# Performance work log

Measured on AMD Instinct MI355X. Metric: run time of the kernel, lower is better.

## Reference

```python
import jax, jax.numpy as jnp
import numpy as np

B, T, D, H = 2, 2048, 1024, 16
DH = D // H  # head dim = 64


def setup_inputs() -> dict:
    key = jax.random.key(0)
    ks = jax.random.split(key, 10)
    s = D ** -0.5
    inp = {
        "x": jax.random.normal(ks[0], (B, T, D), jnp.float32),
        "data_mask": jax.random.randint(ks[1], (B, T), 0, 2, jnp.int32),
        "Wq": jax.random.normal(ks[2], (D, D), jnp.float32) * s,
        "bq": jnp.zeros((D,), jnp.float32),
        "Wk": jax.random.normal(ks[3], (D, D), jnp.float32) * s,
        "bk": jnp.zeros((D,), jnp.float32),
        "Wv": jax.random.normal(ks[4], (D, D), jnp.float32) * s,
        "bv": jnp.zeros((D,), jnp.float32),
        "Wp": jax.random.normal(ks[5], (D, D), jnp.float32) * s,
        "bp": jnp.zeros((D,), jnp.float32),
    }
    return inp


def _split_heads(t):
    # [B, T, D] -> [B, H, T, DH]
    return jnp.swapaxes(t.reshape(B, T, H, DH), 1, 2)


def reference(x, data_mask, Wq, bq, Wk, bk, Wv, bv, Wp, bp):
    q = _split_heads(x @ Wq + bq)
    k = _split_heads(x @ Wk + bk)  # kv = x (self-attention)
    v = _split_heads(x @ Wv + bv)

    # combined mask: causal tri AND data_mask outer product -> [B, 1, T, T]
    dm = data_mask.astype(bool)
    causal = jnp.tril(jnp.ones((T, T), bool))
    mask = causal[None, None] & (dm[:, None, :, None] & dm[:, None, None, :])

    q = q * (DH ** -0.5)  # scale_logits
    scores = jnp.einsum('bhqd,bhkd->bhqk', q, k)  # [B, H, T, T]
    scores = jnp.where(mask, scores, -jnp.inf)
    weights = jax.nn.softmax(scores, axis=-1)
    weights = jnp.nan_to_num(weights)  # fully-masked rows -> 0
    o = jnp.einsum('bhqk,bhkd->bhqd', weights, v)

    # recover shape: [B, H, T, DH] -> [B, T, D]
    o = jnp.swapaxes(o, 1, 2).reshape(B, T, D)
    o = o @ Wp + bp

    # linear mask: multiply output by data_mask [B, T, 1]
    o = o * data_mask.astype(o.dtype)[..., None]
    return o
```

## Files before the change

kernel.cpp:

```cpp
#include <hip/hip_runtime.h>
#include <hip/hip_bf16.h>
#include <cstdint>
#include <cstddef>

#define Bb 2
#define Tt 2048
#define Dd 1024
#define Hh 16
#define DHh 64

using short8 = __attribute__((ext_vector_type(8))) short;
using f32x4  = __attribute__((ext_vector_type(4))) float;
typedef unsigned short u16;

__device__ __forceinline__ u16 f2bf(float f) {
    unsigned int u = __float_as_uint(f);
    u += 0x7fffu + ((u >> 16) & 1u);
    return (u16)(u >> 16);
}

__device__ __forceinline__ unsigned int pk2bf(float a, float b) {
    union { __hip_bfloat162 h; unsigned int u; } c;
    c.h = __float22bfloat162_rn(float2{a, b});
    return c.u;
}

__device__ __forceinline__ void gload16(const void* g, void* l) {
    __builtin_amdgcn_global_load_lds((const __attribute__((address_space(1))) void*)g,
                                     (__attribute__((address_space(3))) void*)l, 16, 0, 0);
}

__device__ __forceinline__ void gemm_bt_core(const u16* __restrict__ A, const u16* __restrict__ BT,
                                             int K, int m0, int n0,
                                             u16* As, u16* Bs, f32x4 acc[4][4]) {
    const int tid = threadIdx.x;
    const int w = tid >> 6, lane = tid & 63;
    const int lr = lane & 15, lg = lane >> 4;
    const int wr = w >> 1, wc = w & 1;
    const int arow = lane >> 2;
    const int acol = (lane & 3) * 8;
    for (int kk = 0; kk < K; kk += 32) {
        __syncthreads();
#pragma unroll
        for (int j = 0; j < 2; ++j) {
            int r0 = w * 32 + j * 16;
            gload16(A  + (size_t)(m0 + r0 + arow) * K + kk + acol, (char*)As + r0 * 64);
            gload16(BT + (size_t)(n0 + r0 + arow) * K + kk + acol, (char*)Bs + r0 * 64);
        }
        __syncthreads();
        short8 af[4], bfv[4];
#pragma unroll
        for (int m = 0; m < 4; ++m)
            af[m] = *(const short8*)((const char*)As + ((wr * 64 + m * 16 + lr) * 64 + lg * 16));
#pragma unroll
        for (int n = 0; n < 4; ++n)
            bfv[n] = *(const short8*)((const char*)Bs + ((wc * 64 + n * 16 + lr) * 64 + lg * 16));
#pragma unroll
        for (int m = 0; m < 4; ++m)
#pragma unroll
            for (int n = 0; n < 4; ++n)
                acc[m][n] = __builtin_amdgcn_mfma_f32_16x16x32_bf16(af[m], bfv[n], acc[m][n], 0, 0, 0);
    }
}

__global__ __launch_bounds__(256) void convert_x_k(const float4* __restrict__ x4,
                                                   ushort4* __restrict__ xb4, int n4,
                                                   const int* __restrict__ dmask,
                                                   float* __restrict__ dmb) {
    int i = blockIdx.x * 256 + threadIdx.x;
    if (i < n4) {
        float4 v = x4[i];
        ushort4 o;
        o.x = f2bf(v.x); o.y = f2bf(v.y); o.z = f2bf(v.z); o.w = f2bf(v.w);
        xb4[i] = o;
    }
    if (i < Bb * Tt) dmb[i] = dmask[i] ? 0.f : -15000.f;
}

__global__ void transpose_w_k(const float* __restrict__ Wq, const float* __restrict__ Wk,
                              const float* __restrict__ Wv, const float* __restrict__ Wp,
                              u16* __restrict__ wt) {
    __shared__ float tile[32][33];
    const int z = blockIdx.z;
    const float* W = (z == 0) ? Wq : (z == 1) ? Wk : (z == 2) ? Wv : Wp;
    const int n0 = blockIdx.x * 32, k0 = blockIdx.y * 32;
    const int tx = threadIdx.x, ty = threadIdx.y;
#pragma unroll
    for (int j = 0; j < 4; ++j)
        tile[ty + j * 8][tx] = W[(size_t)(k0 + ty + j * 8) * Dd + n0 + tx];
    __syncthreads();
    u16* outp = wt + (size_t)z * Dd * Dd;
#pragma unroll
    for (int j = 0; j < 4; ++j)
        outp[(size_t)(n0 + ty + j * 8) * Dd + k0 + tx] = f2bf(tile[tx][ty + j * 8]);
}

__global__ __launch_bounds__(256) void qkv_gemm_k(const u16* __restrict__ xb, const u16* __restrict__ wt,
        const float* __restrict__ bq, const float* __restrict__ bk, const float* __restrict__ bv,
        u16* __restrict__ Qg, u16* __restrict__ Kg, u16* __restrict__ VTg) {
    __shared__ alignas(16) u16 As[128 * 32];
    __shared__ alignas(16) u16 Bs[128 * 32];
    f32x4 acc[4][4];
    const f32x4 vzero = {0.f, 0.f, 0.f, 0.f};
#pragma unroll
    for (int m = 0; m < 4; ++m)
#pragma unroll
        for (int n = 0; n < 4; ++n) acc[m][n] = vzero;
    const int m0 = blockIdx.y * 128, n0 = blockIdx.x * 128;
    gemm_bt_core(xb, wt, 1024, m0, n0, As, Bs, acc);
    const int tid = threadIdx.x, w = tid >> 6, lane = tid & 63, lr = lane & 15, lg = lane >> 4;
    const int wr = w >> 1, wc = w & 1;
    const int sec = n0 >> 10;
    const float* bias = (sec == 0) ? bq : (sec == 1) ? bk : bv;
    u16* dst = (sec == 0) ? Qg : (sec == 1) ? Kg : VTg;
    const float qscale = (sec == 0) ? 0.125f * 1.4426950408889634f : 1.0f;
#pragma unroll
    for (int n = 0; n < 4; ++n) {
        int gn = n0 + wc * 64 + n * 16 + lr;
        int j = gn & 1023;
        float bj = bias[j];
        int h = j >> 6, dh = j & 63;
#pragma unroll
        for (int m = 0; m < 4; ++m) {
            int gmb = m0 + wr * 64 + m * 16 + 4 * lg;
#pragma unroll
            for (int i = 0; i < 4; ++i) {
                int gm = gmb + i;
                int b = gm >> 11, t = gm & 2047;
                float v = (acc[m][n][i] + bj) * qscale;
                size_t off;
                if (sec < 2) off = (((size_t)(b * Hh + h)) * Tt + t) * DHh + dh;
                else {
                    int kt2 = t >> 7, a = t & 127;
                    int ks2 = a >> 5, r = a & 31;
                    int pos = ks2 * 32 + ((r & 15) >> 2) * 8 + ((r >> 4) & 1) * 4 + (r & 3);
                    int chunkp = (pos >> 3) ^ (dh & 7);
                    off = (((size_t)(b * Hh + h) * 16 + kt2) * 64 + dh) * 128 + chunkp * 8 + (pos & 7);
                }
                dst[off] = f2bf(v);
            }
        }
    }
}

__global__ __launch_bounds__(256, 4) void attn_k(const u16* __restrict__ Qg, const u16* __restrict__ Kg,
        const u16* __restrict__ VTg, const float* __restrict__ dmb, u16* __restrict__ Og) {
    __shared__ alignas(16) u16 Ks[128 * 64];
    __shared__ alignas(16) u16 Vs[64 * 128];
    const int bh = blockIdx.x;
    const int qb = (int)gridDim.y - 1 - (int)blockIdx.y;
    const int b = bh >> 4, h = bh & 15;
    const int tid = threadIdx.x, w = tid >> 6, lane = tid & 63;
    const int lr = lane & 15, lg = lane >> 4;
    const int q0 = qb * 64 + w * 16;
    const int qrow = q0 + lr;
    const u16* Qbase = Qg + ((size_t)bh * Tt + q0) * DHh;
    short8 qf0 = *(const short8*)(Qbase + lr * DHh + lg * 8);
    short8 qf1 = *(const short8*)(Qbase + lr * DHh + 32 + lg * 8);
    const f32x4 vzero = {0.f, 0.f, 0.f, 0.f};
    const short8 ones8 = {(short)0x3F80, (short)0x3F80, (short)0x3F80, (short)0x3F80,
                          (short)0x3F80, (short)0x3F80, (short)0x3F80, (short)0x3F80};
    f32x4 o[4];
#pragma unroll
    for (int n = 0; n < 4; ++n) o[n] = vzero;
    f32x4 acc_l = vzero;
    const int ktiles = (qb * 64 + 63) / 128 + 1;
    char* KsB = (char*)Ks; char* VsB = (char*)Vs;

    for (int kt = 0; kt < ktiles; ++kt) {
        const int kbase = kt * 128;
        __syncthreads();
#pragma unroll
        for (int j = 0; j < 4; ++j) {
            int r0 = w * 32 + j * 8;
            int r = r0 + (lane >> 3);
            int cs = (lane & 7) ^ (r & 7);
            gload16(Kg + ((size_t)bh * Tt + kbase + r) * DHh + cs * 8, KsB + r0 * 128);
        }
        {
            const u16* vsrc = VTg + (((size_t)bh * 16 + kt) * 8192) + w * 2048 + lane * 8;
#pragma unroll
            for (int j = 0; j < 4; ++j)
                gload16(vsrc + j * 512, VsB + w * 4096 + j * 1024);
        }
        __syncthreads();
        f32x4 s[8];
        const float* bb = dmb + (size_t)b * Tt + kbase + 4 * lg;
#pragma unroll
        for (int nf = 0; nf < 8; ++nf) {
            int r = nf * 16 + lr;
            short8 k0v = *(const short8*)(KsB + r * 128 + (((0 + lg) ^ (r & 7)) << 4));
            short8 k1v = *(const short8*)(KsB + r * 128 + (((4 + lg) ^ (r & 7)) << 4));
            f32x4 cin = *(const f32x4*)(bb + nf * 16);
            f32x4 t0 = __builtin_amdgcn_mfma_f32_16x16x32_bf16(k0v, qf0, cin, 0, 0, 0);
            s[nf] = __builtin_amdgcn_mfma_f32_16x16x32_bf16(k1v, qf1, t0, 0, 0, 0);
        }
        if (kbase + 127 > q0) {
#pragma unroll
            for (int nf = 0; nf < 8; ++nf) {
                int tk = kbase + 16 * nf + 4 * lg;
#pragma unroll
                for (int i = 0; i < 4; ++i)
                    if (tk + i > qrow) s[nf][i] -= 15000.f;
            }
        }
#pragma unroll
        for (int ks = 0; ks < 4; ++ks) {
            union { uint4 u; short8 sv; } pf;
            pf.u.x = pk2bf(exp2f(s[2 * ks][0]), exp2f(s[2 * ks][1]));
            pf.u.y = pk2bf(exp2f(s[2 * ks][2]), exp2f(s[2 * ks][3]));
            pf.u.z = pk2bf(exp2f(s[2 * ks + 1][0]), exp2f(s[2 * ks + 1][1]));
            pf.u.w = pk2bf(exp2f(s[2 * ks + 1][2]), exp2f(s[2 * ks + 1][3]));
            acc_l = __builtin_amdgcn_mfma_f32_16x16x32_bf16(ones8, pf.sv, acc_l, 0, 0, 0);
#pragma unroll
            for (int n = 0; n < 4; ++n) {
                int rv = n * 16 + lr;
                short8 vf = *(const short8*)(VsB + rv * 256 + ((((ks * 4 + lg)) ^ (rv & 7)) << 4));
                o[n] = __builtin_amdgcn_mfma_f32_16x16x32_bf16(vf, pf.sv, o[n], 0, 0, 0);
            }
        }
    }
    float l = acc_l[0];
    float inv = l > 0.f ? 1.0f / l : 0.f;
#pragma unroll
    for (int n = 0; n < 4; ++n) {
        uint2 pw;
        pw.x = pk2bf(o[n][0] * inv, o[n][1] * inv);
        pw.y = pk2bf(o[n][2] * inv, o[n][3] * inv);
        *(uint2*)(Og + ((size_t)(b * Tt + qrow)) * Dd + h * DHh + n * 16 + 4 * lg) = pw;
    }
}

__global__ __launch_bounds__(256) void out_gemm_k(const u16* __restrict__ Og, const u16* __restrict__ wpt,
        const float* __restrict__ bp, const int* __restrict__ dmask, float* __restrict__ out) {
    __shared__ alignas(16) u16 As[128 * 32];
    __shared__ alignas(16) u16 Bs[128 * 32];
    f32x4 acc[4][4];
    const f32x4 vzero = {0.f, 0.f, 0.f, 0.f};
#pragma unroll
    for (int m = 0; m < 4; ++m)
#pragma unroll
        for (int n = 0; n < 4; ++n) acc[m][n] = vzero;
    const int m0 = blockIdx.y * 128, n0 = blockIdx.x * 128;
    gemm_bt_core(Og, wpt, 1024, m0, n0, As, Bs, acc);
    const int tid = threadIdx.x, w = tid >> 6, lane = tid & 63, lr = lane & 15, lg = lane >> 4;
    const int wr = w >> 1, wc = w & 1;
#pragma unroll
    for (int n = 0; n < 4; ++n) {
        int gn = n0 + wc * 64 + n * 16 + lr;
        float bj = bp[gn];
#pragma unroll
        for (int m = 0; m < 4; ++m) {
            int gmb = m0 + wr * 64 + m * 16 + 4 * lg;
#pragma unroll
            for (int i = 0; i < 4; ++i) {
                int gm = gmb + i;
                float dmv = (float)dmask[gm];
                out[(size_t)gm * Dd + gn] = (acc[m][n][i] + bj) * dmv;
            }
        }
    }
}

extern "C" void kernel_launch(void* const* d_in, const int* in_sizes, int n_in,
                              void* d_out, int out_size, void* d_ws, size_t ws_size,
                              hipStream_t stream) {
    const float* x   = (const float*)d_in[0];
    const int*  dmask = (const int*)d_in[1];
    const float* Wq = (const float*)d_in[2];
    const float* bq = (const float*)d_in[3];
    const float* Wk = (const float*)d_in[4];
    const float* bk = (const float*)d_in[5];
    const float* Wv = (const float*)d_in[6];
    const float* bv = (const float*)d_in[7];
    const float* Wp = (const float*)d_in[8];
    const float* bp = (const float*)d_in[9];
    float* out = (float*)d_out;
    char* ws = (char*)d_ws;
    u16* xb  = (u16*)(ws);
    u16* wt  = (u16*)(ws + ((size_t)8 << 20));
    u16* Qg  = (u16*)(ws + ((size_t)16 << 20));
    u16* Kg  = (u16*)(ws + ((size_t)24 << 20));
    u16* VTg = (u16*)(ws + ((size_t)32 << 20));
    float* dmb = (float*)(ws + ((size_t)40 << 20));
    u16* Og  = xb;

    convert_x_k<<<dim3(4096), dim3(256), 0, stream>>>((const float4*)x, (ushort4*)xb,
                                                      (Bb * Tt * Dd) / 4, dmask, dmb);
    transpose_w_k<<<dim3(32, 32, 4), dim3(32, 8), 0, stream>>>(Wq, Wk, Wv, Wp, wt);
    qkv_gemm_k<<<dim3(24, 32), dim3(256), 0, stream>>>(xb, wt, bq, bk, bv, Qg, Kg, VTg);
    attn_k<<<dim3(32, 32), dim3(256), 0, stream>>>(Qg, Kg, VTg, dmb, Og);
    out_gemm_k<<<dim3(8, 32), dim3(256), 0, stream>>>(Og, wt + (size_t)3 * Dd * Dd, bp, dmask, out);
}
```

Before: 113.7 us.

## Process two 64-row query blocks per attention workgroup to reuse K/V tiles

Each attention workgroup now handles 128 query rows, with every wave owning two 16-row query fragments 64 rows apart, so each K/V tile loaded into LDS feeds twice as many MFMAs. The grid's query dimension is halved and launch bounds drop to 2 waves-per-EU occupancy to allow the doubled register state. This cuts global/LDS K/V traffic and sync overhead per query. The trade-offs are lower occupancy, fewer blocks for load balancing across CUs, and some wasted work on masked rows in the diagonal tile.

```diff
diff --git a/kernel.cpp b/kernel.cpp
--- a/kernel.cpp
+++ b/kernel.cpp
@@ -143,7 +143,7 @@
     }
 }
 
-__global__ __launch_bounds__(256, 4) void attn_k(const u16* __restrict__ Qg, const u16* __restrict__ Kg,
+__global__ __launch_bounds__(256, 2) void attn_k(const u16* __restrict__ Qg, const u16* __restrict__ Kg,
         const u16* __restrict__ VTg, const float* __restrict__ dmb, u16* __restrict__ Og) {
     __shared__ alignas(16) u16 Ks[128 * 64];
     __shared__ alignas(16) u16 Vs[64 * 128];
@@ -152,19 +152,23 @@
     const int b = bh >> 4, h = bh & 15;
     const int tid = threadIdx.x, w = tid >> 6, lane = tid & 63;
     const int lr = lane & 15, lg = lane >> 4;
-    const int q0 = qb * 64 + w * 16;
-    const int qrow = q0 + lr;
-    const u16* Qbase = Qg + ((size_t)bh * Tt + q0) * DHh;
-    short8 qf0 = *(const short8*)(Qbase + lr * DHh + lg * 8);
-    short8 qf1 = *(const short8*)(Qbase + lr * DHh + 32 + lg * 8);
+    const int q0 = qb * 128 + w * 16;
+    const int q1 = q0 + 64;
+    const int qrow0 = q0 + lr, qrow1 = q1 + lr;
+    const u16* Qb0 = Qg + ((size_t)bh * Tt + qrow0) * DHh;
+    const u16* Qb1 = Qg + ((size_t)bh * Tt + qrow1) * DHh;
+    short8 qf0a = *(const short8*)(Qb0 + lg * 8);
+    short8 qf1a = *(const short8*)(Qb0 + 32 + lg * 8);
+    short8 qf0b = *(const short8*)(Qb1 + lg * 8);
+    short8 qf1b = *(const short8*)(Qb1 + 32 + lg * 8);
     const f32x4 vzero = {0.f, 0.f, 0.f, 0.f};
     const short8 ones8 = {(short)0x3F80, (short)0x3F80, (short)0x3F80, (short)0x3F80,
                           (short)0x3F80, (short)0x3F80, (short)0x3F80, (short)0x3F80};
-    f32x4 o[4];
-#pragma unroll
-    for (int n = 0; n < 4; ++n) o[n] = vzero;
-    f32x4 acc_l = vzero;
-    const int ktiles = (qb * 64 + 63) / 128 + 1;
+    f32x4 oa[4], ob[4];
+#pragma unroll
+    for (int n = 0; n < 4; ++n) { oa[n] = vzero; ob[n] = vzero; }
+    f32x4 acc_la = vzero, acc_lb = vzero;
+    const int ktiles = qb + 1;
     char* KsB = (char*)Ks; char* VsB = (char*)Vs;
 
     for (int kt = 0; kt < ktiles; ++kt) {
@@ -184,7 +188,7 @@
                 gload16(vsrc + j * 512, VsB + w * 4096 + j * 1024);
         }
         __syncthreads();
-        f32x4 s[8];
+        f32x4 sa[8], sb[8];
         const float* bb = dmb + (size_t)b * Tt + kbase + 4 * lg;
 #pragma unroll
         for (int nf = 0; nf < 8; ++nf) {
@@ -192,42 +196,56 @@
             short8 k0v = *(const short8*)(KsB + r * 128 + (((0 + lg) ^ (r & 7)) << 4));
             short8 k1v = *(const short8*)(KsB + r * 128 + (((4 + lg) ^ (r & 7)) << 4));
             f32x4 cin = *(const f32x4*)(bb + nf * 16);
-            f32x4 t0 = __builtin_amdgcn_mfma_f32_16x16x32_bf16(k0v, qf0, cin, 0, 0, 0);
-            s[nf] = __builtin_amdgcn_mfma_f32_16x16x32_bf16(k1v, qf1, t0, 0, 0, 0);
-        }
-        if (kbase + 127 > q0) {
+            f32x4 t0a = __builtin_amdgcn_mfma_f32_16x16x32_bf16(k0v, qf0a, cin, 0, 0, 0);
+            sa[nf] = __builtin_amdgcn_mfma_f32_16x16x32_bf16(k1v, qf1a, t0a, 0, 0, 0);
+            f32x4 t0b = __builtin_amdgcn_mfma_f32_16x16x32_bf16(k0v, qf0b, cin, 0, 0, 0);
+            sb[nf] = __builtin_amdgcn_mfma_f32_16x16x32_bf16(k1v, qf1b, t0b, 0, 0, 0);
+        }
+        if (kt == qb) {
 #pragma unroll
             for (int nf = 0; nf < 8; ++nf) {
                 int tk = kbase + 16 * nf + 4 * lg;
 #pragma unroll
-                for (int i = 0; i < 4; ++i)
-                    if (tk + i > qrow) s[nf][i] -= 15000.f;
+                for (int i = 0; i < 4; ++i) {
+                    if (tk + i > qrow0) sa[nf][i] -= 15000.f;
+                    if (tk + i > qrow1) sb[nf][i] -= 15000.f;
+                }
             }
         }
 #pragma unroll
         for (int ks = 0; ks < 4; ++ks) {
-            union { uint4 u; short8 sv; } pf;
-            pf.u.x = pk2bf(exp2f(s[2 * ks][0]), exp2f(s[2 * ks][1]));
-            pf.u.y = pk2bf(exp2f(s[2 * ks][2]), exp2f(s[2 * ks][3]));
-            pf.u.z = pk2bf(exp2f(s[2 * ks + 1][0]), exp2f(s[2 * ks + 1][1]));
-            pf.u.w = pk2bf(exp2f(s[2 * ks + 1][2]), exp2f(s[2 * ks + 1][3]));
-            acc_l = __builtin_amdgcn_mfma_f32_16x16x32_bf16(ones8, pf.sv, acc_l, 0, 0, 0);
+            union { uint4 u; short8 sv; } pfa, pfb;
+            pfa.u.x = pk2bf(exp2f(sa[2 * ks][0]), exp2f(sa[2 * ks][1]));
+            pfa.u.y = pk2bf(exp2f(sa[2 * ks][2]), exp2f(sa[2 * ks][3]));
+            pfa.u.z = pk2bf(exp2f(sa[2 * ks + 1][0]), exp2f(sa[2 * ks + 1][1]));
+            pfa.u.w = pk2bf(exp2f(sa[2 * ks + 1][2]), exp2f(sa[2 * ks + 1][3]));
+            pfb.u.x = pk2bf(exp2f(sb[2 * ks][0]), exp2f(sb[2 * ks][1]));
+            pfb.u.y = pk2bf(exp2f(sb[2 * ks][2]), exp2f(sb[2 * ks][3]));
+            pfb.u.z = pk2bf(exp2f(sb[2 * ks + 1][0]), exp2f(sb[2 * ks + 1][1]));
+            pfb.u.w = pk2bf(exp2f(sb[2 * ks + 1][2]), exp2f(sb[2 * ks + 1][3]));
+            acc_la = __builtin_amdgcn_mfma_f32_16x16x32_bf16(ones8, pfa.sv, acc_la, 0, 0, 0);
+            acc_lb = __builtin_amdgcn_mfma_f32_16x16x32_bf16(ones8, pfb.sv, acc_lb, 0, 0, 0);
 #pragma unroll
             for (int n = 0; n < 4; ++n) {
                 int rv = n * 16 + lr;
                 short8 vf = *(const short8*)(VsB + rv * 256 + ((((ks * 4 + lg)) ^ (rv & 7)) << 4));
-                o[n] = __builtin_amdgcn_mfma_f32_16x16x32_bf16(vf, pf.sv, o[n], 0, 0, 0);
+                oa[n] = __builtin_amdgcn_mfma_f32_16x16x32_bf16(vf, pfa.sv, oa[n], 0, 0, 0);
+                ob[n] = __builtin_amdgcn_mfma_f32_16x16x32_bf16(vf, pfb.sv, ob[n], 0, 0, 0);
             }
         }
     }
-    float l = acc_l[0];
-    float inv = l > 0.f ? 1.0f / l : 0.f;
+    float la = acc_la[0], lb = acc_lb[0];
+    float inva = la > 0.f ? 1.0f / la : 0.f;
+    float invb = lb > 0.f ? 1.0f / lb : 0.f;
 #pragma unroll
     for (int n = 0; n < 4; ++n) {
         uint2 pw;
-        pw.x = pk2bf(o[n][0] * inv, o[n][1] * inv);
-        pw.y = pk2bf(o[n][2] * inv, o[n][3] * inv);
-        *(uint2*)(Og + ((size_t)(b * Tt + qrow)) * Dd + h * DHh + n * 16 + 4 * lg) = pw;
+        pw.x = pk2bf(oa[n][0] * inva, oa[n][1] * inva);
+        pw.y = pk2bf(oa[n][2] * inva, oa[n][3] * inva);
+        *(uint2*)(Og + ((size_t)(b * Tt + qrow0)) * Dd + h * DHh + n * 16 + 4 * lg) = pw;
+        pw.x = pk2bf(ob[n][0] * invb, ob[n][1] * invb);
+        pw.y = pk2bf(ob[n][2] * invb, ob[n][3] * invb);
+        *(uint2*)(Og + ((size_t)(b * Tt + qrow1)) * Dd + h * DHh + n * 16 + 4 * lg) = pw;
     }
 }
 
@@ -289,6 +307,6 @@
                                                       (Bb * Tt * Dd) / 4, dmask, dmb);
     transpose_w_k<<<dim3(32, 32, 4), dim3(32, 8), 0, stream>>>(Wq, Wk, Wv, Wp, wt);
     qkv_gemm_k<<<dim3(24, 32), dim3(256), 0, stream>>>(xb, wt, bq, bk, bv, Qg, Kg, VTg);
-    attn_k<<<dim3(32, 32), dim3(256), 0, stream>>>(Qg, Kg, VTg, dmb, Og);
+    attn_k<<<dim3(32, 16), dim3(256), 0, stream>>>(Qg, Kg, VTg, dmb, Og);
     out_gemm_k<<<dim3(8, 32), dim3(256), 0, stream>>>(Og, wt + (size_t)3 * Dd * Dd, bp, dmask, out);
 }
```

Result: slower. 125.8 us (+10.6%).

## Double-buffer K/V tiles in LDS for attention kernel

Applied to the files above, without the earlier changes.

The attention kernel now keeps two LDS buffers for the K and V tiles. It issues the global-to-LDS loads for the next key tile before computing on the current one, so only one barrier per iteration remains. The aim is to overlap memory latency with the MFMA and exp work. In exchange, LDS use per block doubles and launch bounds drop from 4 to 2 blocks per CU, which lowers occupancy and the latency hiding that came from running more waves.

```diff
diff --git a/kernel.cpp b/kernel.cpp
--- a/kernel.cpp
+++ b/kernel.cpp
@@ -143,10 +143,10 @@
     }
 }
 
-__global__ __launch_bounds__(256, 4) void attn_k(const u16* __restrict__ Qg, const u16* __restrict__ Kg,
+__global__ __launch_bounds__(256, 2) void attn_k(const u16* __restrict__ Qg, const u16* __restrict__ Kg,
         const u16* __restrict__ VTg, const float* __restrict__ dmb, u16* __restrict__ Og) {
-    __shared__ alignas(16) u16 Ks[128 * 64];
-    __shared__ alignas(16) u16 Vs[64 * 128];
+    __shared__ alignas(16) u16 Ks[2][128 * 64];
+    __shared__ alignas(16) u16 Vs[2][64 * 128];
     const int bh = blockIdx.x;
     const int qb = (int)gridDim.y - 1 - (int)blockIdx.y;
     const int b = bh >> 4, h = bh & 15;
@@ -165,25 +165,31 @@
     for (int n = 0; n < 4; ++n) o[n] = vzero;
     f32x4 acc_l = vzero;
     const int ktiles = (qb * 64 + 63) / 128 + 1;
-    char* KsB = (char*)Ks; char* VsB = (char*)Vs;
-
+
+#define STAGEKV(BUF, KT) do { \
+    const int kb_ = (KT) * 128; \
+    _Pragma("unroll") \
+    for (int j_ = 0; j_ < 4; ++j_) { \
+        int r0_ = w * 32 + j_ * 8; \
+        int r_ = r0_ + (lane >> 3); \
+        int cs_ = (lane & 7) ^ (r_ & 7); \
+        gload16(Kg + ((size_t)bh * Tt + kb_ + r_) * DHh + cs_ * 8, (char*)&Ks[BUF][0] + r0_ * 128); \
+    } \
+    { \
+        const u16* vsrc_ = VTg + (((size_t)bh * 16 + (KT)) * 8192) + w * 2048 + lane * 8; \
+        _Pragma("unroll") \
+        for (int j_ = 0; j_ < 4; ++j_) \
+            gload16(vsrc_ + j_ * 512, (char*)&Vs[BUF][0] + w * 4096 + j_ * 1024); \
+    } } while (0)
+
+    STAGEKV(0, 0);
+    __syncthreads();
+    int buf = 0;
     for (int kt = 0; kt < ktiles; ++kt) {
         const int kbase = kt * 128;
-        __syncthreads();
-#pragma unroll
-        for (int j = 0; j < 4; ++j) {
-            int r0 = w * 32 + j * 8;
-            int r = r0 + (lane >> 3);
-            int cs = (lane & 7) ^ (r & 7);
-            gload16(Kg + ((size_t)bh * Tt + kbase + r) * DHh + cs * 8, KsB + r0 * 128);
-        }
-        {
-            const u16* vsrc = VTg + (((size_t)bh * 16 + kt) * 8192) + w * 2048 + lane * 8;
-#pragma unroll
-            for (int j = 0; j < 4; ++j)
-                gload16(vsrc + j * 512, VsB + w * 4096 + j * 1024);
-        }
-        __syncthreads();
+        if (kt + 1 < ktiles) { if (buf) STAGEKV(0, kt + 1); else STAGEKV(1, kt + 1); }
+        const char* KsB = (const char*)&Ks[buf][0];
+        const char* VsB = (const char*)&Vs[buf][0];
         f32x4 s[8];
         const float* bb = dmb + (size_t)b * Tt + kbase + 4 * lg;
 #pragma unroll
@@ -219,7 +225,10 @@
                 o[n] = __builtin_amdgcn_mfma_f32_16x16x32_bf16(vf, pf.sv, o[n], 0, 0, 0);
             }
         }
-    }
+        __syncthreads();
+        buf ^= 1;
+    }
+#undef STAGEKV
     float l = acc_l[0];
     float inv = l > 0.f ? 1.0f / l : 0.f;
 #pragma unroll
```

Result: no change. 115.2 us (+1.3%).
